# Kernel optimization log

Hardware: AMD Instinct MI355X
Metric: run time of the kernel (lower is better)

The kernel has to match this reference:

```python
import jax, jax.numpy as jnp
import numpy as np

H = 4      # SSM / attn heads (d_model/headdim = 256/64)
WIN = 4    # attention window over bands


def _ln(x, g, b):
    m = jnp.mean(x, -1, keepdims=True)
    v = jnp.mean((x - m) ** 2, -1, keepdims=True)
    return (x - m) * jax.lax.rsqrt(v + 1e-5) * g + b


def setup_inputs() -> dict:
    key = jax.random.key(0)
    ks = jax.random.split(key, 24)
    def rn(i, shape, s=0.05):
        return jax.random.normal(ks[i], shape, jnp.float32) * s
    B, T, K, D = 2, 256, 8, 256
    return {
        "z": rn(0, (B, T, K, D), 1.0),
        "ln1_g": jnp.ones((D,), jnp.float32), "ln1_b": jnp.zeros((D,), jnp.float32),
        "Wx": rn(1, (D, D)), "conv_w": rn(2, (D, 4), 0.3), "Wz": rn(3, (D, D)),
        "Wb": rn(4, (D, H * 128)), "Wc": rn(5, (D, H * 128)), "Wdt": rn(6, (D, H)),
        "dt_bias": rn(7, (H,), 0.5), "A_log": rn(8, (H,), 0.5), "theta": rn(9, (H,), 1.0),
        "D_skip": rn(10, (H,), 1.0), "mimo_U": rn(11, (H, H), 0.5), "mimo_V": rn(12, (H, H), 0.5),
        "Wout": rn(13, (D, D)),
        "ln2_g": jnp.ones((D,), jnp.float32), "ln2_b": jnp.zeros((D,), jnp.float32),
        "attn_in_w": rn(14, (3 * D, D)), "attn_in_b": rn(15, (3 * D,), 0.02),
        "attn_out_w": rn(16, (D, D)), "attn_out_b": jnp.zeros((D,), jnp.float32),
        "ln3_g": jnp.ones((D,), jnp.float32), "ln3_b": jnp.zeros((D,), jnp.float32),
        "Wg": rn(17, (D, 4 * D)), "Wu": rn(18, (D, 4 * D)), "Wd": rn(19, (4 * D, D)),
    }


def _forward(z, ln1_g, ln1_b, Wx, conv_w, Wz, Wb, Wc, Wdt, dt_bias, A_log, theta,
             D_skip, mimo_U, mimo_V, Wout, ln2_g, ln2_b, attn_in_w, attn_in_b,
             attn_out_w, attn_out_b, ln3_g, ln3_b, Wg, Wu, Wd):
    B, T, K, D = z.shape
    P = D // H
    N = Wb.shape[1] // H
    # ---------- (a) intra-band Mamba3 (complex MIMO selective scan) ----------
    u = _ln(z, ln1_g, ln1_b)
    u = jnp.transpose(u, (0, 2, 1, 3)).reshape(B * K, T, D)   # [BK,T,D]
    x = u @ Wx
    # causal depthwise conv1d, kernel 4
    xp = jnp.pad(x, ((0, 0), (3, 0), (0, 0)))
    x = sum(xp[:, k:k + T, :] * conv_w[:, k] for k in range(4))
    x = jax.nn.silu(x)
    xh = x.reshape(B * K, T, H, P)
    Bm = (u @ Wb).reshape(B * K, T, H, N)
    Cm = (u @ Wc).reshape(B * K, T, H, N)
    Mmix = mimo_U @ mimo_V.T                                  # rank-r cross-head coupling
    Bm = jnp.einsum('hg,btgn->bthn', Mmix, Bm)
    dt = jax.nn.softplus(u @ Wdt + dt_bias)                   # [BK,T,H]
    A = -jnp.exp(A_log)                                       # stable real decay
    mag = jnp.exp(dt * A)
    ph = dt * theta                                           # harmonic rotation
    ar, ai = mag * jnp.cos(ph), mag * jnp.sin(ph)
    xs = tuple(jnp.moveaxis(t, 1, 0) for t in (xh, Bm, Cm, dt, ar, ai))
    h0 = jnp.zeros((B * K, H, N, P), x.dtype)

    def step(carry, s):
        h_re, h_im = carry
        xt, bt, ct, dtt, art, ait = s
        dBx = (dtt[:, :, None, None] * bt[:, :, :, None]) * xt[:, :, None, :]
        nr = art[:, :, None, None] * h_re - ait[:, :, None, None] * h_im + dBx
        ni = art[:, :, None, None] * h_im + ait[:, :, None, None] * h_re
        return (nr, ni), jnp.einsum('bhn,bhnp->bhp', ct, nr)   # Re(C . h)

    _, ys = jax.lax.scan(step, (h0, h0), xs)                  # ys: [T,BK,H,P]
    y = jnp.moveaxis(ys, 0, 1) + D_skip[None, None, :, None] * xh
    y = y.reshape(B * K, T, D) * jax.nn.silu(u @ Wz)
    y = y @ Wout
    z = z + jnp.transpose(y.reshape(B, K, T, D), (0, 2, 1, 3))
    # ---------- (b) inter-band windowed attention ----------
    zn = _ln(z, ln2_g, ln2_b).reshape(B * T, K, D)
    qkv = zn @ attn_in_w.T + attn_in_b
    q, k_, v = jnp.split(qkv, 3, axis=-1)
    hd = D // H
    def hs(t):
        return t.reshape(B * T, K // WIN, WIN, H, hd).transpose(0, 1, 3, 2, 4)
    q, k_, v = hs(q), hs(k_), hs(v)
    s = jnp.einsum('mwhqd,mwhkd->mwhqk', q, k_) * jnp.float32(1.0 / np.sqrt(hd))
    a = jax.nn.softmax(s, axis=-1)
    o = jnp.einsum('mwhqk,mwhkd->mwhqd', a, v).transpose(0, 1, 3, 2, 4).reshape(B * T, K, D)
    z = z + (o @ attn_out_w.T + attn_out_b).reshape(B, T, K, D)
    # ---------- (c) SwiGLU FFN ----------
    zf = _ln(z, ln3_g, ln3_b)
    z = z + (jax.nn.silu(zf @ Wg) * (zf @ Wu)) @ Wd
    return z


def reference(z, ln1_g, ln1_b, Wx, conv_w, Wz, Wb, Wc, Wdt, dt_bias, A_log, theta,
              D_skip, mimo_U, mimo_V, Wout, ln2_g, ln2_b, attn_in_w, attn_in_b,
              attn_out_w, attn_out_b, ln3_g, ln3_b, Wg, Wu, Wd):
    return _forward(z, ln1_g, ln1_b, Wx, conv_w, Wz, Wb, Wc, Wdt, dt_bias, A_log,
                    theta, D_skip, mimo_U, mimo_V, Wout, ln2_g, ln2_b, attn_in_w,
                    attn_in_b, attn_out_w, attn_out_b, ln3_g, ln3_b, Wg, Wu, Wd)
```

## Files before the change

### kernel.cpp

```cpp
#include <hip/hip_runtime.h>
#include <hip/hip_bf16.h>
#include <math.h>

typedef __hip_bfloat16 bf16;
typedef __attribute__((ext_vector_type(8))) short s16x8;
typedef __attribute__((ext_vector_type(4))) float f32x4;

__device__ __forceinline__ float siluf(float x) { return x / (1.f + __expf(-x)); }
__device__ __forceinline__ float bits2f(unsigned short u) {
    union { float f; unsigned i; } v; v.i = ((unsigned)u) << 16; return v.f;
}
__device__ __forceinline__ unsigned short f2bits(float f) {
    return (unsigned short)__bfloat16_as_ushort(__float2bfloat16(f));
}

#define KFL 1024
#define OFF_UB   (768*KFL)
#define OFF_DTV  (1280*KFL)
#define OFF_BMB  (1344*KFL)
#define OFF_CMB  (2368*KFL)
#define OFF_ZGB  (3392*KFL)
#define OFF_XB   (3904*KFL)
#define OFF_X2T  (4928*KFL)
#define OFF_P    (5440*KFL)
#define OFF_YGB  (7488*KFL)
#define OFF_Z1   (8000*KFL)
#define OFF_ZNB  OFF_UB
#define OFF_QKV  OFF_BMB
#define OFF_OB   (2880*KFL)
#define OFF_Z2   OFF_P
#define OFF_ZFB  (6464*KFL)
#define OFF_GG   OFF_BMB

#define W_BCZX 0
#define W_OUT  393216
#define W_QKV  458752
#define W_AO   655360
#define W_GU   720896
#define W_D    1245184

__global__ __launch_bounds__(256) void prep_ln1_kernel(
    const float* __restrict__ Wx, const float* __restrict__ Wb,
    const float* __restrict__ Wc, const float* __restrict__ Wz,
    const float* __restrict__ Wo, const float* __restrict__ Wqkv,
    const float* __restrict__ Wao, const float* __restrict__ Wg,
    const float* __restrict__ Wu, const float* __restrict__ Wd,
    const float* __restrict__ U, const float* __restrict__ V,
    unsigned short* __restrict__ wout,
    const float* __restrict__ z, const float* __restrict__ g1,
    const float* __restrict__ b1, const float* __restrict__ Wdt,
    const float* __restrict__ dt_bias,
    unsigned short* __restrict__ u, float4* __restrict__ dtv4)
{
    __shared__ __align__(16) float smem[64 * 65];
    int blk = blockIdx.x;
    int tid = threadIdx.x;
    if (blk < 368) {
        if (blk >= 304) {
            int off = blk - 304;
            const float* src; int dst, base;
            if (off < 48) { src = Wqkv; dst = W_QKV; base = off * 4096; }
            else          { src = Wao;  dst = W_AO;  base = (off - 48) * 4096; }
            #pragma unroll
            for (int i = 0; i < 16; i++) {
                int idx = base + tid + i * 256;
                wout[dst + idx] = f2bits(src[idx]);
            }
            return;
        }
        float* lds = smem;
        const float* src; int srcN, n0, sc0, k0, dstoff, dstK, mix = 0, t;
        if (blk < 32)       { t = blk;       src = Wb; srcN = 512;  dstoff = W_BCZX; dstK = 256;
                              n0 = (t >> 2) * 64;        sc0 = 0; k0 = (t & 3) * 64; mix = 1; }
        else if (blk < 64)  { t = blk - 32;  src = Wc; srcN = 512;  dstoff = W_BCZX; dstK = 256;
                              n0 = 512 + (t >> 2) * 64;  sc0 = (t >> 2) * 64; k0 = (t & 3) * 64; }
        else if (blk < 80)  { t = blk - 64;  src = Wz; srcN = 256;  dstoff = W_BCZX; dstK = 256;
                              n0 = 1024 + (t >> 2) * 64; sc0 = (t >> 2) * 64; k0 = (t & 3) * 64; }
        else if (blk < 96)  { t = blk - 80;  src = Wx; srcN = 256;  dstoff = W_BCZX; dstK = 256;
                              n0 = 1280 + (t >> 2) * 64; sc0 = (t >> 2) * 64; k0 = (t & 3) * 64; }
        else if (blk < 112) { t = blk - 96;  src = Wo; srcN = 256;  dstoff = W_OUT;  dstK = 256;
                              n0 = (t >> 2) * 64;        sc0 = n0; k0 = (t & 3) * 64; }
        else if (blk < 176) { t = blk - 112; src = Wg; srcN = 1024; dstoff = W_GU;   dstK = 256;
                              n0 = (t >> 2) * 64;        sc0 = n0; k0 = (t & 3) * 64; }
        else if (blk < 240) { t = blk - 176; src = Wu; srcN = 1024; dstoff = W_GU;   dstK = 256;
                              n0 = 1024 + (t >> 2) * 64; sc0 = (t >> 2) * 64; k0 = (t & 3) * 64; }
        else                { t = blk - 240; src = Wd; srcN = 256;  dstoff = W_D;    dstK = 1024;
                              n0 = (t >> 4) * 64;        sc0 = n0; k0 = (t & 15) * 64; }
        if (mix) {
            int h = n0 >> 7, scol = n0 & 127;
            float mm[4];
            #pragma unroll
            for (int g = 0; g < 4; g++) {
                float s = 0.f;
                #pragma unroll
                for (int j = 0; j < 4; j++) s += U[h * 4 + j] * V[g * 4 + j];
                mm[g] = s;
            }
            #pragma unroll
            for (int i = 0; i < 16; i++) {
                int idx = tid + i * 256;
                int kk = idx >> 6, nn = idx & 63;
                const float* row = src + (size_t)(k0 + kk) * 512 + scol + nn;
                lds[kk * 65 + nn] = mm[0] * row[0] + mm[1] * row[128]
                                  + mm[2] * row[256] + mm[3] * row[384];
            }
        } else {
            #pragma unroll
            for (int i = 0; i < 16; i++) {
                int idx = tid + i * 256;
                int kk = idx >> 6, nn = idx & 63;
                lds[kk * 65 + nn] = src[(size_t)(k0 + kk) * srcN + sc0 + nn];
            }
        }
        __syncthreads();
// ... 268 lines not shown
            int s = bx * 128 + nwave + nf * 16 + lq;
            float ms = mAs[s];
            float ps = phs[s];
            float ds = dss[s];
            #pragma unroll
            for (int r = 0; r < 4; r++) {
                float wgt = (s <= tg[r])
                    ? __expf(tmv[r] - ms) * __cosf(tpv[r] - ps) * ds : 0.f;
                Pout[tg[r] * 256 + s] = f2bits(acc[mf][nf][r] * wgt);
            }
        }
    }
}

__global__ __launch_bounds__(256) void gemm_y(
    const unsigned short* __restrict__ P, const unsigned short* __restrict__ x2t,
    const unsigned short* __restrict__ zgb, const float* __restrict__ Dsk,
    unsigned short* __restrict__ ygb)
{
    int by = blockIdx.x, bh = blockIdx.y;
    int bk = bh >> 2, h = bh & 3;
    int tid = threadIdx.x;
    int w = tid >> 6, l = tid & 63;
    int mw = (w >> 1) * 32, nw = (w & 1) * 32;
    int lq = l & 15, lh = l >> 4;
    __shared__ __align__(16) unsigned short As[64 * 72];
    __shared__ __align__(16) unsigned short Bs[64 * 72];
    f32x4 acc[2][2] = {};
    int srow = tid >> 3, sc = (tid & 7) * 8;
    const unsigned short* Ap = P + (size_t)bh * 65536 + (size_t)(by * 64 + srow) * 256 + sc;
    const unsigned short* Bp = x2t + (size_t)bh * 16384 + (size_t)srow * 256 + sc;
    int kmax = (by + 1) * 64; if (kmax > 256) kmax = 256;
    uint4 a0 = *(const uint4*)(Ap);
    uint4 a1 = *(const uint4*)(Ap + (size_t)32 * 256);
    uint4 b0 = *(const uint4*)(Bp);
    uint4 b1 = *(const uint4*)(Bp + (size_t)32 * 256);
    for (int k0 = 0; k0 < kmax; k0 += 64) {
        if (k0) __syncthreads();
        *(uint4*)&As[srow * 72 + sc] = a0;
        *(uint4*)&As[(srow + 32) * 72 + sc] = a1;
        *(uint4*)&Bs[srow * 72 + sc] = b0;
        *(uint4*)&Bs[(srow + 32) * 72 + sc] = b1;
        __syncthreads();
        if (k0 + 64 < kmax) {
            a0 = *(const uint4*)(Ap + k0 + 64);
            a1 = *(const uint4*)(Ap + (size_t)32 * 256 + k0 + 64);
            b0 = *(const uint4*)(Bp + k0 + 64);
            b1 = *(const uint4*)(Bp + (size_t)32 * 256 + k0 + 64);
        }
        #pragma unroll
        for (int kk = 0; kk < 2; kk++) {
            int kof = kk * 32 + lh * 8;
            s16x8 bfr[2];
            #pragma unroll
            for (int nf = 0; nf < 2; nf++)
                bfr[nf] = *(const s16x8*)&Bs[(nw + nf * 16 + lq) * 72 + kof];
            #pragma unroll
            for (int mf = 0; mf < 2; mf++) {
                s16x8 af = *(const s16x8*)&As[(mw + mf * 16 + lq) * 72 + kof];
                #pragma unroll
                for (int nf = 0; nf < 2; nf++)
                    acc[mf][nf] = __builtin_amdgcn_mfma_f32_16x16x32_bf16(af, bfr[nf], acc[mf][nf], 0, 0, 0);
            }
        }
    }
    float dsk = Dsk[h];
    #pragma unroll
    for (int mf = 0; mf < 2; mf++) {
        #pragma unroll
        for (int nf = 0; nf < 2; nf++) {
            int p = nw + nf * 16 + lq;
            #pragma unroll
            for (int r = 0; r < 4; r++) {
                int t = by * 64 + mw + mf * 16 + lh * 4 + r;
                float xv = bits2f(x2t[(size_t)bh * 16384 + p * 256 + t]);
                float zg = bits2f(zgb[(size_t)(bk * 256 + t) * 256 + h * 64 + p]);
                ygb[(size_t)(bk * 256 + t) * 256 + h * 64 + p] =
                    f2bits((acc[mf][nf][r] + dsk * xv) * zg);
            }
        }
    }
}

__global__ __launch_bounds__(256) void gemm_ln(
    const unsigned short* __restrict__ A, const unsigned short* __restrict__ Bt,
    const float* __restrict__ bias, const float* __restrict__ resid,
    const float* __restrict__ g, const float* __restrict__ b,
    float* __restrict__ zfull, unsigned short* __restrict__ znorm, int rowmap)
{
    const int K = 256;
    __shared__ __align__(16) unsigned short As[16 * 72];
    __shared__ __align__(16) unsigned short Bs[256 * 72];
    __shared__ float partS[16][4], partQ[16][4];
    int tid = threadIdx.x;
    int m0 = blockIdx.x * 16;
    int w = tid >> 6, l = tid & 63;
    int nw = w * 64;
    int lq = l & 15, lh = l >> 4;
    f32x4 acc[4] = {};
    int srow = tid >> 3, sc = (tid & 7) * 8;
    const unsigned short* Ap = A + (size_t)(m0 + (srow & 15)) * K + sc;
    const unsigned short* Bp = Bt + (size_t)srow * K + sc;
    uint4 a0 = *(const uint4*)(Ap);
    uint4 b0 = *(const uint4*)(Bp);
    uint4 b1 = *(const uint4*)(Bp + (size_t)32 * K);
    uint4 b2 = *(const uint4*)(Bp + (size_t)64 * K);
    uint4 b3 = *(const uint4*)(Bp + (size_t)96 * K);
    uint4 b4 = *(const uint4*)(Bp + (size_t)128 * K);
    uint4 b5 = *(const uint4*)(Bp + (size_t)160 * K);
    uint4 b6 = *(const uint4*)(Bp + (size_t)192 * K);
    uint4 b7 = *(const uint4*)(Bp + (size_t)224 * K);
    for (int k0 = 0; k0 < K; k0 += 64) {
        if (k0) __syncthreads();
        if (tid < 128) *(uint4*)&As[srow * 72 + sc] = a0;
        *(uint4*)&Bs[srow * 72 + sc] = b0;
        *(uint4*)&Bs[(srow + 32) * 72 + sc] = b1;
        *(uint4*)&Bs[(srow + 64) * 72 + sc] = b2;
        *(uint4*)&Bs[(srow + 96) * 72 + sc] = b3;
        *(uint4*)&Bs[(srow + 128) * 72 + sc] = b4;
        *(uint4*)&Bs[(srow + 160) * 72 + sc] = b5;
        *(uint4*)&Bs[(srow + 192) * 72 + sc] = b6;
        *(uint4*)&Bs[(srow + 224) * 72 + sc] = b7;
        __syncthreads();
        if (k0 + 64 < K) {
            a0 = *(const uint4*)(Ap + k0 + 64);
            b0 = *(const uint4*)(Bp + k0 + 64);
            b1 = *(const uint4*)(Bp + (size_t)32 * K + k0 + 64);
            b2 = *(const uint4*)(Bp + (size_t)64 * K + k0 + 64);
            b3 = *(const uint4*)(Bp + (size_t)96 * K + k0 + 64);
            b4 = *(const uint4*)(Bp + (size_t)128 * K + k0 + 64);
            b5 = *(const uint4*)(Bp + (size_t)160 * K + k0 + 64);
            b6 = *(const uint4*)(Bp + (size_t)192 * K + k0 + 64);
            b7 = *(const uint4*)(Bp + (size_t)224 * K + k0 + 64);
        }
        #pragma unroll
        for (int kk = 0; kk < 2; kk++) {
            int kof = kk * 32 + lh * 8;
            s16x8 af = *(const s16x8*)&As[lq * 72 + kof];
            #pragma unroll
            for (int nf = 0; nf < 4; nf++) {
                s16x8 bf = *(const s16x8*)&Bs[(nw + nf * 16 + lq) * 72 + kof];
                acc[nf] = __builtin_amdgcn_mfma_f32_16x16x32_bf16(af, bf, acc[nf], 0, 0, 0);
            }
        }
    }
    float bv[4];
    #pragma unroll
    for (int nf = 0; nf < 4; nf++) bv[nf] = bias ? bias[nw + nf * 16 + lq] : 0.f;
    int orow[4];
    #pragma unroll
    for (int r = 0; r < 4; r++) {
        int rb = m0 + lh * 4 + r;
        if (rowmap) {
            int bk = rb >> 8, t = rb & 255;
            orow[r] = ((bk >> 3) * 256 + t) * 8 + (bk & 7);
        } else orow[r] = rb;
    }
    #pragma unroll
    for (int r = 0; r < 4; r++) {
        float s = 0.f, q = 0.f;
        #pragma unroll
        for (int nf = 0; nf < 4; nf++) {
            float v = acc[nf][r] + bv[nf]
                    + resid[(size_t)orow[r] * 256 + nw + nf * 16 + lq];
            acc[nf][r] = v;
            s += v; q += v * v;
        }
        #pragma unroll
        for (int off = 1; off < 16; off <<= 1) {
            s += __shfl_xor(s, off, 64);
            q += __shfl_xor(q, off, 64);
        }
        if (lq == 0) {
            int row = lh * 4 + r;
            partS[row][w] = s; partQ[row][w] = q;
        }
    }
    __syncthreads();
    float gv[4], bbv[4];
    #pragma unroll
    for (int nf = 0; nf < 4; nf++) {
        gv[nf] = g[nw + nf * 16 + lq];
        bbv[nf] = b[nw + nf * 16 + lq];
    }
    #pragma unroll
    for (int r = 0; r < 4; r++) {
        int row = lh * 4 + r;
        float sum = partS[row][0] + partS[row][1] + partS[row][2] + partS[row][3];
        float sq  = partQ[row][0] + partQ[row][1] + partQ[row][2] + partQ[row][3];
        float mean = sum * (1.f / 256.f);
        float var = sq * (1.f / 256.f) - mean * mean;
        float rstd = rsqrtf(var + 1e-5f);
        size_t ro = (size_t)orow[r] * 256;
        #pragma unroll
        for (int nf = 0; nf < 4; nf++) {
            int n = nw + nf * 16 + lq;
            float v = acc[nf][r];
            zfull[ro + n] = v;
            znorm[ro + n] = f2bits((v - mean) * rstd * gv[nf] + bbv[nf]);
        }
    }
}

__global__ __launch_bounds__(256) void mfma_gemm(
    const unsigned short* __restrict__ A, const unsigned short* __restrict__ Bt,
    const float* __restrict__ bias, void* __restrict__ C,
    int N, int K, int out_bf16)
{
    __shared__ __align__(16) unsigned short As[128 * 72];
    __shared__ __align__(16) unsigned short Bs[128 * 72];
    int tid = threadIdx.x;
    int n0 = blockIdx.x * 128, m0 = blockIdx.y * 128;
    int w = tid >> 6, l = tid & 63;
    int mwave = (w >> 1) * 64, nwave = (w & 1) * 64;
    f32x4 acc[4][4] = {};
    int srow = tid >> 3, sc = (tid & 7) * 8;
    const unsigned short* Ap = A + (size_t)(m0 + srow) * K + sc;
    const unsigned short* Bp = Bt + (size_t)(n0 + srow) * K + sc;
    int lq = l & 15, lh = l >> 4;
    uint4 a0 = *(const uint4*)(Ap);
    uint4 a1 = *(const uint4*)(Ap + (size_t)32 * K);
    uint4 a2 = *(const uint4*)(Ap + (size_t)64 * K);
    uint4 a3 = *(const uint4*)(Ap + (size_t)96 * K);
    uint4 b0 = *(const uint4*)(Bp);
    uint4 b1 = *(const uint4*)(Bp + (size_t)32 * K);
    uint4 b2 = *(const uint4*)(Bp + (size_t)64 * K);
    uint4 b3 = *(const uint4*)(Bp + (size_t)96 * K);
    for (int k0 = 0; k0 < K; k0 += 64) {
        if (k0) __syncthreads();
        *(uint4*)&As[srow * 72 + sc] = a0;
        *(uint4*)&As[(srow + 32) * 72 + sc] = a1;
        *(uint4*)&As[(srow + 64) * 72 + sc] = a2;
        *(uint4*)&As[(srow + 96) * 72 + sc] = a3;
        *(uint4*)&Bs[srow * 72 + sc] = b0;
        *(uint4*)&Bs[(srow + 32) * 72 + sc] = b1;
        *(uint4*)&Bs[(srow + 64) * 72 + sc] = b2;
        *(uint4*)&Bs[(srow + 96) * 72 + sc] = b3;
        __syncthreads();
        if (k0 + 64 < K) {
            a0 = *(const uint4*)(Ap + k0 + 64);
            a1 = *(const uint4*)(Ap + (size_t)32 * K + k0 + 64);
            a2 = *(const uint4*)(Ap + (size_t)64 * K + k0 + 64);
            a3 = *(const uint4*)(Ap + (size_t)96 * K + k0 + 64);
            b0 = *(const uint4*)(Bp + k0 + 64);
            b1 = *(const uint4*)(Bp + (size_t)32 * K + k0 + 64);
            b2 = *(const uint4*)(Bp + (size_t)64 * K + k0 + 64);
            b3 = *(const uint4*)(Bp + (size_t)96 * K + k0 + 64);
        }
        #pragma unroll
        for (int kk = 0; kk < 2; kk++) {
            int kof = kk * 32 + lh * 8;
            s16x8 bfr[4];
            #pragma unroll
            for (int nf = 0; nf < 4; nf++)
                bfr[nf] = *(const s16x8*)&Bs[(nwave + nf * 16 + lq) * 72 + kof];
            #pragma unroll
            for (int mf = 0; mf < 4; mf++) {
                s16x8 af = *(const s16x8*)&As[(mwave + mf * 16 + lq) * 72 + kof];
                #pragma unroll
                for (int nf = 0; nf < 4; nf++)
                    acc[mf][nf] = __builtin_amdgcn_mfma_f32_16x16x32_bf16(af, bfr[nf], acc[mf][nf], 0, 0, 0);
            }
        }
    }
    #pragma unroll
    for (int mf = 0; mf < 4; mf++) {
        #pragma unroll
        for (int nf = 0; nf < 4; nf++) {
            int n = n0 + nwave + nf * 16 + lq;
            float bs_ = bias ? bias[n] : 0.f;
            #pragma unroll
            for (int r = 0; r < 4; r++) {
                int m = m0 + mwave + mf * 16 + lh * 4 + r;
                float v = acc[mf][nf][r] + bs_;
                if (out_bf16) ((unsigned short*)C)[(size_t)m * N + n] = f2bits(v);
                else          ((float*)C)[(size_t)m * N + n] = v;
            }
        }
    }
}

__global__ __launch_bounds__(256) void gemm_gu2(
    const unsigned short* __restrict__ A, const unsigned short* __restrict__ Wgu,
    unsigned short* __restrict__ gg)
{
    const int K = 256;
    __shared__ __align__(16) unsigned short As[128 * 72];
    __shared__ __align__(16) unsigned short Bgs[64 * 72];
    __shared__ __align__(16) unsigned short Bus[64 * 72];
    int tid = threadIdx.x;
    int n0 = blockIdx.x * 64, m0 = blockIdx.y * 128;
    int w = tid >> 6, l = tid & 63;
    int mwave = (w >> 1) * 64, nwave = (w & 1) * 32;
    int lq = l & 15, lh = l >> 4;
    f32x4 ag[4][2] = {}, au[4][2] = {};
    int srow = tid >> 3, sc = (tid & 7) * 8;
    const unsigned short* Ap = A + (size_t)(m0 + srow) * K + sc;
    const unsigned short* Bgp = Wgu + (size_t)(n0 + srow) * K + sc;
    const unsigned short* Bup = Wgu + (size_t)(1024 + n0 + srow) * K + sc;
    uint4 a0 = *(const uint4*)(Ap);
    uint4 a1 = *(const uint4*)(Ap + (size_t)32 * K);
    uint4 a2 = *(const uint4*)(Ap + (size_t)64 * K);
    uint4 a3 = *(const uint4*)(Ap + (size_t)96 * K);
    uint4 bg0 = *(const uint4*)(Bgp);
    uint4 bg1 = *(const uint4*)(Bgp + (size_t)32 * K);
    uint4 bu0 = *(const uint4*)(Bup);
    uint4 bu1 = *(const uint4*)(Bup + (size_t)32 * K);
    for (int k0 = 0; k0 < K; k0 += 64) {
        if (k0) __syncthreads();
        *(uint4*)&As[srow * 72 + sc] = a0;
        *(uint4*)&As[(srow + 32) * 72 + sc] = a1;
        *(uint4*)&As[(srow + 64) * 72 + sc] = a2;
        *(uint4*)&As[(srow + 96) * 72 + sc] = a3;
        *(uint4*)&Bgs[srow * 72 + sc] = bg0;
        *(uint4*)&Bgs[(srow + 32) * 72 + sc] = bg1;
        *(uint4*)&Bus[srow * 72 + sc] = bu0;
        *(uint4*)&Bus[(srow + 32) * 72 + sc] = bu1;
        __syncthreads();
        if (k0 + 64 < K) {
            a0 = *(const uint4*)(Ap + k0 + 64);
            a1 = *(const uint4*)(Ap + (size_t)32 * K + k0 + 64);
            a2 = *(const uint4*)(Ap + (size_t)64 * K + k0 + 64);
            a3 = *(const uint4*)(Ap + (size_t)96 * K + k0 + 64);
            bg0 = *(const uint4*)(Bgp + k0 + 64);
            bg1 = *(const uint4*)(Bgp + (size_t)32 * K + k0 + 64);
            bu0 = *(const uint4*)(Bup + k0 + 64);
            bu1 = *(const uint4*)(Bup + (size_t)32 * K + k0 + 64);
        }
        #pragma unroll
        for (int kk = 0; kk < 2; kk++) {
            int kof = kk * 32 + lh * 8;
            s16x8 bgr[2], bur[2];
            #pragma unroll
            for (int nf = 0; nf < 2; nf++) {
                bgr[nf] = *(const s16x8*)&Bgs[(nwave + nf * 16 + lq) * 72 + kof];
                bur[nf] = *(const s16x8*)&Bus[(nwave + nf * 16 + lq) * 72 + kof];
            }
            #pragma unroll
            for (int mf = 0; mf < 4; mf++) {
                s16x8 af = *(const s16x8*)&As[(mwave + mf * 16 + lq) * 72 + kof];
                #pragma unroll
                for (int nf = 0; nf < 2; nf++) {
                    ag[mf][nf] = __builtin_amdgcn_mfma_f32_16x16x32_bf16(af, bgr[nf], ag[mf][nf], 0, 0, 0);
                    au[mf][nf] = __builtin_amdgcn_mfma_f32_16x16x32_bf16(af, bur[nf], au[mf][nf], 0, 0, 0);
                }
            }
        }
    }
    #pragma unroll
    for (int mf = 0; mf < 4; mf++) {
        #pragma unroll
        for (int nf = 0; nf < 2; nf++) {
            int n = n0 + nwave + nf * 16 + lq;
            #pragma unroll
            for (int r = 0; r < 4; r++) {
                int m = m0 + mwave + mf * 16 + lh * 4 + r;
                gg[(size_t)m * 1024 + n] = f2bits(siluf(ag[mf][nf][r]) * au[mf][nf][r]);
            }
        }
    }
}

__global__ __launch_bounds__(256) void gemm_d2(
    const unsigned short* __restrict__ gg, const unsigned short* __restrict__ Bt,
    const float* __restrict__ resid, float* __restrict__ out)
{
    __shared__ __align__(16) unsigned short As[64 * 72];
    __shared__ __align__(16) unsigned short Bs[64 * 72];
    const int K = 1024, N = 256;
    int tid = threadIdx.x;
    int n0 = blockIdx.x * 64, m0 = blockIdx.y * 64;
    int w = tid >> 6, l = tid & 63;
    int mw = (w >> 1) * 32, nw = (w & 1) * 32;
    f32x4 acc[2][2] = {};
    int srow = tid >> 3, sc = (tid & 7) * 8;
    const unsigned short* Ap = gg + (size_t)(m0 + srow) * K + sc;
    const unsigned short* Bp = Bt + (size_t)(n0 + srow) * K + sc;
    int lq = l & 15, lh = l >> 4;
    uint4 a0 = *(const uint4*)(Ap);
    uint4 a1 = *(const uint4*)(Ap + (size_t)32 * K);
    uint4 b0 = *(const uint4*)(Bp);
    uint4 b1 = *(const uint4*)(Bp + (size_t)32 * K);
    for (int k0 = 0; k0 < K; k0 += 64) {
        if (k0) __syncthreads();
        *(uint4*)&As[srow * 72 + sc] = a0;
        *(uint4*)&As[(srow + 32) * 72 + sc] = a1;
        *(uint4*)&Bs[srow * 72 + sc] = b0;
        *(uint4*)&Bs[(srow + 32) * 72 + sc] = b1;
        __syncthreads();
        if (k0 + 64 < K) {
            a0 = *(const uint4*)(Ap + k0 + 64);
            a1 = *(const uint4*)(Ap + (size_t)32 * K + k0 + 64);
            b0 = *(const uint4*)(Bp + k0 + 64);
            b1 = *(const uint4*)(Bp + (size_t)32 * K + k0 + 64);
        }
        #pragma unroll
        for (int kk = 0; kk < 2; kk++) {
            int kof = kk * 32 + lh * 8;
            s16x8 bfr[2];
            #pragma unroll
            for (int nf = 0; nf < 2; nf++)
                bfr[nf] = *(const s16x8*)&Bs[(nw + nf * 16 + lq) * 72 + kof];
            #pragma unroll
            for (int mf = 0; mf < 2; mf++) {
                s16x8 af = *(const s16x8*)&As[(mw + mf * 16 + lq) * 72 + kof];
                #pragma unroll
                for (int nf = 0; nf < 2; nf++)
                    acc[mf][nf] = __builtin_amdgcn_mfma_f32_16x16x32_bf16(af, bfr[nf], acc[mf][nf], 0, 0, 0);
            }
        }
    }
    #pragma unroll
    for (int mf = 0; mf < 2; mf++) {
        #pragma unroll
        for (int nf = 0; nf < 2; nf++) {
            int n = n0 + nw + nf * 16 + lq;
            #pragma unroll
            for (int r = 0; r < 4; r++) {
                int m = m0 + mw + mf * 16 + lh * 4 + r;
                out[(size_t)m * N + n] = acc[mf][nf][r] + resid[(size_t)m * N + n];
            }
        }
    }
}

__global__ __launch_bounds__(256) void attn_kernel(const unsigned short* __restrict__ qkv,
    unsigned short* __restrict__ o)
{
    int m = blockIdx.x >> 1, w = blockIdx.x & 1;
    int tid = threadIdx.x;
    int h = tid >> 6, d = tid & 63;
    __shared__ float qs[4][256], ks[4][256], vs[4][256];
    #pragma unroll
    for (int j = 0; j < 4; j++) {
        int row = m * 8 + w * 4 + j;
        int base = row * 768;
        qs[j][tid] = bits2f(qkv[base + tid]);
        ks[j][tid] = bits2f(qkv[base + 256 + tid]);
        vs[j][tid] = bits2f(qkv[base + 512 + tid]);
    }
    __syncthreads();
    float sc[4][4];
    #pragma unroll
    for (int qi = 0; qi < 4; qi++)
        #pragma unroll
        for (int ki = 0; ki < 4; ki++) {
            float v = qs[qi][h * 64 + d] * ks[ki][h * 64 + d];
            #pragma unroll
            for (int off = 32; off; off >>= 1) v += __shfl_xor(v, off, 64);
            sc[qi][ki] = v * 0.125f;
        }
    #pragma unroll
    for (int qi = 0; qi < 4; qi++) {
        float mx = fmaxf(fmaxf(sc[qi][0], sc[qi][1]), fmaxf(sc[qi][2], sc[qi][3]));
        float e0 = __expf(sc[qi][0] - mx), e1 = __expf(sc[qi][1] - mx);
        float e2 = __expf(sc[qi][2] - mx), e3 = __expf(sc[qi][3] - mx);
        float inv = 1.f / (e0 + e1 + e2 + e3);
        float ov = (e0 * vs[0][h * 64 + d] + e1 * vs[1][h * 64 + d] +
                    e2 * vs[2][h * 64 + d] + e3 * vs[3][h * 64 + d]) * inv;
        o[(m * 8 + w * 4 + qi) * 256 + h * 64 + d] = f2bits(ov);
    }
}

extern "C" void kernel_launch(void* const* d_in, const int* in_sizes, int n_in,
                              void* d_out, int out_size, void* d_ws, size_t ws_size,
                              hipStream_t stream)
{
    const float* z         = (const float*)d_in[0];
    const float* ln1_g     = (const float*)d_in[1];
    const float* ln1_b     = (const float*)d_in[2];
    const float* Wx        = (const float*)d_in[3];
    const float* conv_w    = (const float*)d_in[4];
    const float* Wz        = (const float*)d_in[5];
    const float* Wb        = (const float*)d_in[6];
    const float* Wc        = (const float*)d_in[7];
    const float* Wdt       = (const float*)d_in[8];
    const float* dt_bias   = (const float*)d_in[9];
    const float* A_log     = (const float*)d_in[10];
    const float* theta     = (const float*)d_in[11];
    const float* D_skip    = (const float*)d_in[12];
    const float* mimo_U    = (const float*)d_in[13];
    const float* mimo_V    = (const float*)d_in[14];
    const float* Wout      = (const float*)d_in[15];
    const float* ln2_g     = (const float*)d_in[16];
    const float* ln2_b     = (const float*)d_in[17];
    const float* attn_in_w = (const float*)d_in[18];
    const float* attn_in_b = (const float*)d_in[19];
    const float* attn_out_w= (const float*)d_in[20];
    const float* attn_out_b= (const float*)d_in[21];
    const float* ln3_g     = (const float*)d_in[22];
    const float* ln3_b     = (const float*)d_in[23];
    const float* Wg        = (const float*)d_in[24];
    const float* Wu        = (const float*)d_in[25];
    const float* Wd        = (const float*)d_in[26];

    float* W = (float*)d_ws;
    unsigned short* wts = (unsigned short*)W;
    unsigned short* ub  = (unsigned short*)(W + OFF_UB);
    float4* dtv4        = (float4*)(W + OFF_DTV);
    unsigned short* bmb = (unsigned short*)(W + OFF_BMB);
    unsigned short* cmb = (unsigned short*)(W + OFF_CMB);
    unsigned short* zgb = (unsigned short*)(W + OFF_ZGB);
    unsigned short* xb  = (unsigned short*)(W + OFF_XB);
    unsigned short* x2t = (unsigned short*)(W + OFF_X2T);
    unsigned short* pbuf= (unsigned short*)(W + OFF_P);
    unsigned short* ygb = (unsigned short*)(W + OFF_YGB);
    float* z1           = W + OFF_Z1;
    unsigned short* znb = (unsigned short*)(W + OFF_ZNB);
    unsigned short* qkvb= (unsigned short*)(W + OFF_QKV);
    unsigned short* ob  = (unsigned short*)(W + OFF_OB);
    float* z2           = W + OFF_Z2;
    unsigned short* zfb = (unsigned short*)(W + OFF_ZFB);
    unsigned short* gg  = (unsigned short*)(W + OFF_GG);

    prep_ln1_kernel<<<4464, 256, 0, stream>>>(
        Wx, Wb, Wc, Wz, Wout, attn_in_w, attn_out_w, Wg, Wu, Wd, mimo_U, mimo_V,
        wts, z, ln1_g, ln1_b, Wdt, dt_bias, ub, dtv4);
    gemm_bczx<<<dim3(12, 32), 256, 0, stream>>>(ub, wts + W_BCZX, bmb, cmb, zgb, xb);
    s_conv_kernel<<<448, 256, 0, stream>>>(cmb, bmb, dtv4, A_log, theta, pbuf,
                                           xb, conv_w, x2t);
    gemm_y<<<dim3(4, 64), 256, 0, stream>>>(pbuf, x2t, zgb, D_skip, ygb);
    gemm_ln<<<256, 256, 0, stream>>>(ygb, wts + W_OUT, nullptr, z, ln2_g, ln2_b,
                                     z1, znb, 1);
    mfma_gemm<<<dim3(6, 32), 256, 0, stream>>>(znb, wts + W_QKV, attn_in_b, qkvb, 768, 256, 1);
    attn_kernel<<<1024, 256, 0, stream>>>(qkvb, ob);
    gemm_ln<<<256, 256, 0, stream>>>(ob, wts + W_AO, attn_out_b, z1, ln3_g, ln3_b,
                                     z2, zfb, 0);
    gemm_gu2<<<dim3(16, 32), 256, 0, stream>>>(zfb, wts + W_GU, gg);
    gemm_d2<<<dim3(4, 64), 256, 0, stream>>>(gg, wts + W_D, z2, (float*)d_out);
}
```

Measured before the change: 209.9 us.

## Fuse out-proj, LN2, QKV GEMM, band attention, attn-out and LN3 into one kernel

Replaces four launches (gemm_ln, mfma_gemm, attn_kernel, gemm_ln) with one mid_kernel. Each block owns 16 rows, which are two full 8-band tokens, so the windowed attention can run entirely in shared memory. The row permutation moves from the output side to the input gather. This removes the global round trips for z1, the normalized activations, qkv and the attention output, plus three launch gaps. In exchange it uses about 63KB of shared memory per block and runs only 256 blocks, each doing five serialized weight-streaming GEMM passes with many barriers, so occupancy and parallelism drop.

```diff
diff --git a/kernel.cpp b/kernel.cpp
--- a/kernel.cpp
+++ b/kernel.cpp
@@ -24,12 +24,8 @@
 #define OFF_X2T  (4928*KFL)
 #define OFF_P    (5440*KFL)
 #define OFF_YGB  (7488*KFL)
-#define OFF_Z1   (8000*KFL)
-#define OFF_ZNB  OFF_UB
-#define OFF_QKV  OFF_BMB
-#define OFF_OB   (2880*KFL)
-#define OFF_Z2   OFF_P
-#define OFF_ZFB  (6464*KFL)
+#define OFF_Z2   (8000*KFL)
+#define OFF_ZFB  (9024*KFL)
 #define OFF_GG   OFF_BMB
 
 #define W_BCZX 0
@@ -464,199 +460,306 @@
     }
 }
 
-__global__ __launch_bounds__(256) void gemm_ln(
-    const unsigned short* __restrict__ A, const unsigned short* __restrict__ Bt,
-    const float* __restrict__ bias, const float* __restrict__ resid,
-    const float* __restrict__ g, const float* __restrict__ b,
-    float* __restrict__ zfull, unsigned short* __restrict__ znorm, int rowmap)
+__global__ __launch_bounds__(256) void mid_kernel(
+    const unsigned short* __restrict__ ygb, const unsigned short* __restrict__ wts,
+    const float* __restrict__ zin,
+    const float* __restrict__ g2, const float* __restrict__ b2,
+    const float* __restrict__ qbias, const float* __restrict__ obias,
+    const float* __restrict__ g3, const float* __restrict__ b3,
+    float* __restrict__ z2, unsigned short* __restrict__ zfb)
 {
+    __shared__ __align__(16) char smem[64512];
+    unsigned short* Bs = (unsigned short*)smem;
+    unsigned short* As = (unsigned short*)(smem + 36864);
+    unsigned short* zn = (unsigned short*)(smem + 39168);
+    float* z1s = (float*)(smem + 47616);
+    float (*partS)[4] = (float(*)[4])(smem + 64000);
+    float (*partQ)[4] = (float(*)[4])(smem + 64256);
+    unsigned short* qk = (unsigned short*)smem;
+
     const int K = 256;
-    __shared__ __align__(16) unsigned short As[16 * 72];
-    __shared__ __align__(16) unsigned short Bs[256 * 72];
-    __shared__ float partS[16][4], partQ[16][4];
     int tid = threadIdx.x;
     int m0 = blockIdx.x * 16;
     int w = tid >> 6, l = tid & 63;
     int nw = w * 64;
     int lq = l & 15, lh = l >> 4;
-    f32x4 acc[4] = {};
     int srow = tid >> 3, sc = (tid & 7) * 8;
-    const unsigned short* Ap = A + (size_t)(m0 + (srow & 15)) * K + sc;
-    const unsigned short* Bp = Bt + (size_t)srow * K + sc;
-    uint4 a0 = *(const uint4*)(Ap);
-    uint4 b0 = *(const uint4*)(Bp);
-    uint4 b1 = *(const uint4*)(Bp + (size_t)32 * K);
-    uint4 b2 = *(const uint4*)(Bp + (size_t)64 * K);
-    uint4 b3 = *(const uint4*)(Bp + (size_t)96 * K);
-    uint4 b4 = *(const uint4*)(Bp + (size_t)128 * K);
-    uint4 b5 = *(const uint4*)(Bp + (size_t)160 * K);
-    uint4 b6 = *(const uint4*)(Bp + (size_t)192 * K);
-    uint4 b7 = *(const uint4*)(Bp + (size_t)224 * K);
-    for (int k0 = 0; k0 < K; k0 += 64) {
-        if (k0) __syncthreads();
-        if (tid < 128) *(uint4*)&As[srow * 72 + sc] = a0;
-        *(uint4*)&Bs[srow * 72 + sc] = b0;
-        *(uint4*)&Bs[(srow + 32) * 72 + sc] = b1;
-        *(uint4*)&Bs[(srow + 64) * 72 + sc] = b2;
-        *(uint4*)&Bs[(srow + 96) * 72 + sc] = b3;
-        *(uint4*)&Bs[(srow + 128) * 72 + sc] = b4;
-        *(uint4*)&Bs[(srow + 160) * 72 + sc] = b5;
-        *(uint4*)&Bs[(srow + 192) * 72 + sc] = b6;
-        *(uint4*)&Bs[(srow + 224) * 72 + sc] = b7;
-        __syncthreads();
-        if (k0 + 64 < K) {
-            a0 = *(const uint4*)(Ap + k0 + 64);
-            b0 = *(const uint4*)(Bp + k0 + 64);
-            b1 = *(const uint4*)(Bp + (size_t)32 * K + k0 + 64);
-            b2 = *(const uint4*)(Bp + (size_t)64 * K + k0 + 64);
-            b3 = *(const uint4*)(Bp + (size_t)96 * K + k0 + 64);
-            b4 = *(const uint4*)(Bp + (size_t)128 * K + k0 + 64);
-            b5 = *(const uint4*)(Bp + (size_t)160 * K + k0 + 64);
-            b6 = *(const uint4*)(Bp + (size_t)192 * K + k0 + 64);
-            b7 = *(const uint4*)(Bp + (size_t)224 * K + k0 + 64);
-        }
-        #pragma unroll
-        for (int kk = 0; kk < 2; kk++) {
-            int kof = kk * 32 + lh * 8;
-            s16x8 af = *(const s16x8*)&As[lq * 72 + kof];
+
+    {
+        int rb = m0 + (srow & 15);
+        int irow = ((rb >> 11) * 8 + (rb & 7)) * 256 + ((rb >> 3) & 255);
+        const unsigned short* Ap = ygb + (size_t)irow * K + sc;
+        const unsigned short* Bp = wts + W_OUT + (size_t)srow * K + sc;
+        f32x4 acc[4] = {};
+        uint4 a0 = *(const uint4*)(Ap);
+        uint4 c0 = *(const uint4*)(Bp);
+        uint4 c1 = *(const uint4*)(Bp + (size_t)32 * K);
+        uint4 c2 = *(const uint4*)(Bp + (size_t)64 * K);
+        uint4 c3 = *(const uint4*)(Bp + (size_t)96 * K);
+        uint4 c4 = *(const uint4*)(Bp + (size_t)128 * K);
+        uint4 c5 = *(const uint4*)(Bp + (size_t)160 * K);
+        uint4 c6 = *(const uint4*)(Bp + (size_t)192 * K);
+        uint4 c7 = *(const uint4*)(Bp + (size_t)224 * K);
+        for (int k0 = 0; k0 < K; k0 += 64) {
+            if (k0) __syncthreads();
+            if (tid < 128) *(uint4*)&As[srow * 72 + sc] = a0;
+            *(uint4*)&Bs[srow * 72 + sc] = c0;
+            *(uint4*)&Bs[(srow + 32) * 72 + sc] = c1;
+            *(uint4*)&Bs[(srow + 64) * 72 + sc] = c2;
+            *(uint4*)&Bs[(srow + 96) * 72 + sc] = c3;
+            *(uint4*)&Bs[(srow + 128) * 72 + sc] = c4;
+            *(uint4*)&Bs[(srow + 160) * 72 + sc] = c5;
+            *(uint4*)&Bs[(srow + 192) * 72 + sc] = c6;
+            *(uint4*)&Bs[(srow + 224) * 72 + sc] = c7;
+            __syncthreads();
+            if (k0 + 64 < K) {
+                a0 = *(const uint4*)(Ap + k0 + 64);
+                c0 = *(const uint4*)(Bp + k0 + 64);
+                c1 = *(const uint4*)(Bp + (size_t)32 * K + k0 + 64);
+                c2 = *(const uint4*)(Bp + (size_t)64 * K + k0 + 64);
+                c3 = *(const uint4*)(Bp + (size_t)96 * K + k0 + 64);
+                c4 = *(const uint4*)(Bp + (size_t)128 * K + k0 + 64);
+                c5 = *(const uint4*)(Bp + (size_t)160 * K + k0 + 64);
+                c6 = *(const uint4*)(Bp + (size_t)192 * K + k0 + 64);
+                c7 = *(const uint4*)(Bp + (size_t)224 * K + k0 + 64);
+            }
+            #pragma unroll
+            for (int kk = 0; kk < 2; kk++) {
+                int kof = kk * 32 + lh * 8;
+                s16x8 af = *(const s16x8*)&As[lq * 72 + kof];
+                #pragma unroll
+                for (int nf = 0; nf < 4; nf++) {
+                    s16x8 bf = *(const s16x8*)&Bs[(nw + nf * 16 + lq) * 72 + kof];
+                    acc[nf] = __builtin_amdgcn_mfma_f32_16x16x32_bf16(af, bf, acc[nf], 0, 0, 0);
+                }
+            }
+        }
+        #pragma unroll
+        for (int r = 0; r < 4; r++) {
+            int row = lh * 4 + r;
+            float s = 0.f, q = 0.f;
             #pragma unroll
             for (int nf = 0; nf < 4; nf++) {
-                s16x8 bf = *(const s16x8*)&Bs[(nw + nf * 16 + lq) * 72 + kof];
-                acc[nf] = __builtin_amdgcn_mfma_f32_16x16x32_bf16(af, bf, acc[nf], 0, 0, 0);
-            }
-        }
-    }
-    float bv[4];
-    #pragma unroll
-    for (int nf = 0; nf < 4; nf++) bv[nf] = bias ? bias[nw + nf * 16 + lq] : 0.f;
-    int orow[4];
-    #pragma unroll
-    for (int r = 0; r < 4; r++) {
-        int rb = m0 + lh * 4 + r;
-        if (rowmap) {
-            int bk = rb >> 8, t = rb & 255;
-            orow[r] = ((bk >> 3) * 256 + t) * 8 + (bk & 7);
-        } else orow[r] = rb;
-    }
-    #pragma unroll
-    for (int r = 0; r < 4; r++) {
-        float s = 0.f, q = 0.f;
+                float v = acc[nf][r] + zin[(size_t)(m0 + row) * 256 + nw + nf * 16 + lq];
+                acc[nf][r] = v;
+                s += v; q += v * v;
+            }
+            #pragma unroll
+            for (int off = 1; off < 16; off <<= 1) {
+                s += __shfl_xor(s, off, 64);
+                q += __shfl_xor(q, off, 64);
+            }
+            if (lq == 0) { partS[row][w] = s; partQ[row][w] = q; }
+        }
+        __syncthreads();
+        float gv[4], bbv[4];
         #pragma unroll
         for (int nf = 0; nf < 4; nf++) {
-            float v = acc[nf][r] + bv[nf]
-                    + resid[(size_t)orow[r] * 256 + nw + nf * 16 + lq];
-            acc[nf][r] = v;
-            s += v; q += v * v;
-        }
-        #pragma unroll
-        for (int off = 1; off < 16; off <<= 1) {
-            s += __shfl_xor(s, off, 64);
-            q += __shfl_xor(q, off, 64);
-        }
-        if (lq == 0) {
+            gv[nf] = g2[nw + nf * 16 + lq];
+            bbv[nf] = b2[nw + nf * 16 + lq];
+        }
+        #pragma unroll
+        for (int r = 0; r < 4; r++) {
             int row = lh * 4 + r;
-            partS[row][w] = s; partQ[row][w] = q;
-        }
-    }
+            float sum = partS[row][0] + partS[row][1] + partS[row][2] + partS[row][3];
+            float sq  = partQ[row][0] + partQ[row][1] + partQ[row][2] + partQ[row][3];
+            float mean = sum * (1.f / 256.f);
+            float var = sq * (1.f / 256.f) - mean * mean;
+            float rstd = rsqrtf(var + 1e-5f);
+            #pragma unroll
+            for (int nf = 0; nf < 4; nf++) {
+                int n = nw + nf * 16 + lq;
+                float v = acc[nf][r];
+                z1s[row * 256 + n] = v;
+                zn[row * 264 + n] = f2bits((v - mean) * rstd * gv[nf] + bbv[nf]);
+            }
+        }
+    }
+
+    f32x4 aq0[4] = {}, aq1[4] = {}, aq2[4] = {};
+#define QKV_PASS(PIDX, AQ) do { \
+    const unsigned short* Bp2 = wts + W_QKV + (size_t)((PIDX) * 256 + srow) * 256 + sc; \
+    uint4 d0 = *(const uint4*)(Bp2); \
+    uint4 d1 = *(const uint4*)(Bp2 + (size_t)32 * 256); \
+    uint4 d2 = *(const uint4*)(Bp2 + (size_t)64 * 256); \
+    uint4 d3 = *(const uint4*)(Bp2 + (size_t)96 * 256); \
+    uint4 d4 = *(const uint4*)(Bp2 + (size_t)128 * 256); \
+    uint4 d5 = *(const uint4*)(Bp2 + (size_t)160 * 256); \
+    uint4 d6 = *(const uint4*)(Bp2 + (size_t)192 * 256); \
+    uint4 d7 = *(const uint4*)(Bp2 + (size_t)224 * 256); \
+    for (int k0 = 0; k0 < 256; k0 += 64) { \
+        __syncthreads(); \
+        *(uint4*)&Bs[srow * 72 + sc] = d0; \
+        *(uint4*)&Bs[(srow + 32) * 72 + sc] = d1; \
+        *(uint4*)&Bs[(srow + 64) * 72 + sc] = d2; \
+        *(uint4*)&Bs[(srow + 96) * 72 + sc] = d3; \
+        *(uint4*)&Bs[(srow + 128) * 72 + sc] = d4; \
+        *(uint4*)&Bs[(srow + 160) * 72 + sc] = d5; \
+        *(uint4*)&Bs[(srow + 192) * 72 + sc] = d6; \
+        *(uint4*)&Bs[(srow + 224) * 72 + sc] = d7; \
+        __syncthreads(); \
+        if (k0 + 64 < 256) { \
+            d0 = *(const uint4*)(Bp2 + k0 + 64); \
+            d1 = *(const uint4*)(Bp2 + (size_t)32 * 256 + k0 + 64); \
+            d2 = *(const uint4*)(Bp2 + (size_t)64 * 256 + k0 + 64); \
+            d3 = *(const uint4*)(Bp2 + (size_t)96 * 256 + k0 + 64); \
+            d4 = *(const uint4*)(Bp2 + (size_t)128 * 256 + k0 + 64); \
+            d5 = *(const uint4*)(Bp2 + (size_t)160 * 256 + k0 + 64); \
+            d6 = *(const uint4*)(Bp2 + (size_t)192 * 256 + k0 + 64); \
+            d7 = *(const uint4*)(Bp2 + (size_t)224 * 256 + k0 + 64); \
+        } \
+        _Pragma("unroll") \
+        for (int kk = 0; kk < 2; kk++) { \
+            int kof = kk * 32 + lh * 8; \
+            s16x8 af = *(const s16x8*)&zn[lq * 264 + k0 + kof]; \
+            _Pragma("unroll") \
+            for (int nf = 0; nf < 4; nf++) { \
+                s16x8 bf = *(const s16x8*)&Bs[(nw + nf * 16 + lq) * 72 + kof]; \
+                AQ[nf] = __builtin_amdgcn_mfma_f32_16x16x32_bf16(af, bf, AQ[nf], 0, 0, 0); \
+            } \
+        } \
+    } \
+} while (0)
+    QKV_PASS(0, aq0);
+    QKV_PASS(1, aq1);
+    QKV_PASS(2, aq2);
+#undef QKV_PASS
+
     __syncthreads();
-    float gv[4], bbv[4];
-    #pragma unroll
-    for (int nf = 0; nf < 4; nf++) {
-        gv[nf] = g[nw + nf * 16 + lq];
-        bbv[nf] = b[nw + nf * 16 + lq];
-    }
-    #pragma unroll
-    for (int r = 0; r < 4; r++) {
-        int row = lh * 4 + r;
-        float sum = partS[row][0] + partS[row][1] + partS[row][2] + partS[row][3];
-        float sq  = partQ[row][0] + partQ[row][1] + partQ[row][2] + partQ[row][3];
-        float mean = sum * (1.f / 256.f);
-        float var = sq * (1.f / 256.f) - mean * mean;
-        float rstd = rsqrtf(var + 1e-5f);
-        size_t ro = (size_t)orow[r] * 256;
+#define QKV_STORE(PIDX, AQ) do { \
+    _Pragma("unroll") \
+    for (int nf = 0; nf < 4; nf++) { \
+        int n = (PIDX) * 256 + nw + nf * 16 + lq; \
+        float bb = qbias[n]; \
+        _Pragma("unroll") \
+        for (int r = 0; r < 4; r++) \
+            qk[(lh * 4 + r) * 776 + n] = f2bits(AQ[nf][r] + bb); \
+    } \
+} while (0)
+    QKV_STORE(0, aq0);
+    QKV_STORE(1, aq1);
+    QKV_STORE(2, aq2);
+#undef QKV_STORE
+    __syncthreads();
+    {
+        int hh = w;
+        int d = l;
+        #pragma unroll
+        for (int w4 = 0; w4 < 4; w4++) {
+            int r0 = w4 * 4;
+            float qv[4], kv[4], vv[4];
+            #pragma unroll
+            for (int j = 0; j < 4; j++) {
+                qv[j] = bits2f(qk[(r0 + j) * 776 + hh * 64 + d]);
+                kv[j] = bits2f(qk[(r0 + j) * 776 + 256 + hh * 64 + d]);
+                vv[j] = bits2f(qk[(r0 + j) * 776 + 512 + hh * 64 + d]);
+            }
+            float sc_[4][4];
+            #pragma unroll
+            for (int qi = 0; qi < 4; qi++)
+                #pragma unroll
+                for (int ki = 0; ki < 4; ki++) {
+                    float v = qv[qi] * kv[ki];
+                    #pragma unroll
+                    for (int off = 32; off; off >>= 1) v += __shfl_xor(v, off, 64);
+                    sc_[qi][ki] = v * 0.125f;
+                }
+            #pragma unroll
+            for (int qi = 0; qi < 4; qi++) {
+                float mx = fmaxf(fmaxf(sc_[qi][0], sc_[qi][1]), fmaxf(sc_[qi][2], sc_[qi][3]));
+                float e0 = __expf(sc_[qi][0] - mx), e1 = __expf(sc_[qi][1] - mx);
+                float e2 = __expf(sc_[qi][2] - mx), e3 = __expf(sc_[qi][3] - mx);
+                float inv = 1.f / (e0 + e1 + e2 + e3);
+                float ov = (e0 * vv[0] + e1 * vv[1] + e2 * vv[2] + e3 * vv[3]) * inv;
+                zn[(r0 + qi) * 264 + hh * 64 + d] = f2bits(ov);
+            }
+        }
+    }
+
+    {
+        f32x4 ac4[4] = {};
+        const unsigned short* Bp4 = wts + W_AO + (size_t)srow * K + sc;
+        uint4 c0 = *(const uint4*)(Bp4);
+        uint4 c1 = *(const uint4*)(Bp4 + (size_t)32 * K);
+        uint4 c2 = *(const uint4*)(Bp4 + (size_t)64 * K);
+        uint4 c3 = *(const uint4*)(Bp4 + (size_t)96 * K);
+        uint4 c4 = *(const uint4*)(Bp4 + (size_t)128 * K);
+        uint4 c5 = *(const uint4*)(Bp4 + (size_t)160 * K);
+        uint4 c6 = *(const uint4*)(Bp4 + (size_t)192 * K);
+        uint4 c7 = *(const uint4*)(Bp4 + (size_t)224 * K);
+        for (int k0 = 0; k0 < K; k0 += 64) {
+            __syncthreads();
+            *(uint4*)&Bs[srow * 72 + sc] = c0;
+            *(uint4*)&Bs[(srow + 32) * 72 + sc] = c1;
+            *(uint4*)&Bs[(srow + 64) * 72 + sc] = c2;
+            *(uint4*)&Bs[(srow + 96) * 72 + sc] = c3;
+            *(uint4*)&Bs[(srow + 128) * 72 + sc] = c4;
+            *(uint4*)&Bs[(srow + 160) * 72 + sc] = c5;
+            *(uint4*)&Bs[(srow + 192) * 72 + sc] = c6;
+            *(uint4*)&Bs[(srow + 224) * 72 + sc] = c7;
+            __syncthreads();
+            if (k0 + 64 < K) {
+                c0 = *(const uint4*)(Bp4 + k0 + 64);
+                c1 = *(const uint4*)(Bp4 + (size_t)32 * K + k0 + 64);
+                c2 = *(const uint4*)(Bp4 + (size_t)64 * K + k0 + 64);
+                c3 = *(const uint4*)(Bp4 + (size_t)96 * K + k0 + 64);
+                c4 = *(const uint4*)(Bp4 + (size_t)128 * K + k0 + 64);
+                c5 = *(const uint4*)(Bp4 + (size_t)160 * K + k0 + 64);
+                c6 = *(const uint4*)(Bp4 + (size_t)192 * K + k0 + 64);
+                c7 = *(const uint4*)(Bp4 + (size_t)224 * K + k0 + 64);
+            }
+            #pragma unroll
+            for (int kk = 0; kk < 2; kk++) {
+                int kof = kk * 32 + lh * 8;
+                s16x8 af = *(const s16x8*)&zn[lq * 264 + k0 + kof];
+                #pragma unroll
+                for (int nf = 0; nf < 4; nf++) {
+                    s16x8 bf = *(const s16x8*)&Bs[(nw + nf * 16 + lq) * 72 + kof];
+                    ac4[nf] = __builtin_amdgcn_mfma_f32_16x16x32_bf16(af, bf, ac4[nf], 0, 0, 0);
+                }
+            }
+        }
+        float bv[4], gv[4], bbv[4];
         #pragma unroll
         for (int nf = 0; nf < 4; nf++) {
             int n = nw + nf * 16 + lq;
-            float v = acc[nf][r];
-            zfull[ro + n] = v;
-            znorm[ro + n] = f2bits((v - mean) * rstd * gv[nf] + bbv[nf]);
-        }
-    }
-}
-
-__global__ __launch_bounds__(256) void mfma_gemm(
-    const unsigned short* __restrict__ A, const unsigned short* __restrict__ Bt,
-    const float* __restrict__ bias, void* __restrict__ C,
-    int N, int K, int out_bf16)
-{
-    __shared__ __align__(16) unsigned short As[128 * 72];
-    __shared__ __align__(16) unsigned short Bs[128 * 72];
-    int tid = threadIdx.x;
-    int n0 = blockIdx.x * 128, m0 = blockIdx.y * 128;
-    int w = tid >> 6, l = tid & 63;
-    int mwave = (w >> 1) * 64, nwave = (w & 1) * 64;
-    f32x4 acc[4][4] = {};
-    int srow = tid >> 3, sc = (tid & 7) * 8;
-    const unsigned short* Ap = A + (size_t)(m0 + srow) * K + sc;
-    const unsigned short* Bp = Bt + (size_t)(n0 + srow) * K + sc;
-    int lq = l & 15, lh = l >> 4;
-    uint4 a0 = *(const uint4*)(Ap);
-    uint4 a1 = *(const uint4*)(Ap + (size_t)32 * K);
-    uint4 a2 = *(const uint4*)(Ap + (size_t)64 * K);
-    uint4 a3 = *(const uint4*)(Ap + (size_t)96 * K);
-    uint4 b0 = *(const uint4*)(Bp);
-    uint4 b1 = *(const uint4*)(Bp + (size_t)32 * K);
-    uint4 b2 = *(const uint4*)(Bp + (size_t)64 * K);
-    uint4 b3 = *(const uint4*)(Bp + (size_t)96 * K);
-    for (int k0 = 0; k0 < K; k0 += 64) {
-        if (k0) __syncthreads();
-        *(uint4*)&As[srow * 72 + sc] = a0;
-        *(uint4*)&As[(srow + 32) * 72 + sc] = a1;
-        *(uint4*)&As[(srow + 64) * 72 + sc] = a2;
-        *(uint4*)&As[(srow + 96) * 72 + sc] = a3;
-        *(uint4*)&Bs[srow * 72 + sc] = b0;
-        *(uint4*)&Bs[(srow + 32) * 72 + sc] = b1;
-        *(uint4*)&Bs[(srow + 64) * 72 + sc] = b2;
-        *(uint4*)&Bs[(srow + 96) * 72 + sc] = b3;
-        __syncthreads();
-        if (k0 + 64 < K) {
-            a0 = *(const uint4*)(Ap + k0 + 64);
-            a1 = *(const uint4*)(Ap + (size_t)32 * K + k0 + 64);
-            a2 = *(const uint4*)(Ap + (size_t)64 * K + k0 + 64);
-            a3 = *(const uint4*)(Ap + (size_t)96 * K + k0 + 64);
-            b0 = *(const uint4*)(Bp + k0 + 64);
-            b1 = *(const uint4*)(Bp + (size_t)32 * K + k0 + 64);
-            b2 = *(const uint4*)(Bp + (size_t)64 * K + k0 + 64);
-            b3 = *(const uint4*)(Bp + (size_t)96 * K + k0 + 64);
-        }
-        #pragma unroll
-        for (int kk = 0; kk < 2; kk++) {
-            int kof = kk * 32 + lh * 8;
-            s16x8 bfr[4];
-            #pragma unroll
-            for (int nf = 0; nf < 4; nf++)
-                bfr[nf] = *(const s16x8*)&Bs[(nwave + nf * 16 + lq) * 72 + kof];
-            #pragma unroll
-            for (int mf = 0; mf < 4; mf++) {
-                s16x8 af = *(const s16x8*)&As[(mwave + mf * 16 + lq) * 72 + kof];
-                #pragma unroll
-                for (int nf = 0; nf < 4; nf++)
-                    acc[mf][nf] = __builtin_amdgcn_mfma_f32_16x16x32_bf16(af, bfr[nf], acc[mf][nf], 0, 0, 0);
-            }
-        }
-    }
-    #pragma unroll
-    for (int mf = 0; mf < 4; mf++) {
-        #pragma unroll
-        for (int nf = 0; nf < 4; nf++) {
-            int n = n0 + nwave + nf * 16 + lq;
-            float bs_ = bias ? bias[n] : 0.f;
-            #pragma unroll
-            for (int r = 0; r < 4; r++) {
-                int m = m0 + mwave + mf * 16 + lh * 4 + r;
-                float v = acc[mf][nf][r] + bs_;
-                if (out_bf16) ((unsigned short*)C)[(size_t)m * N + n] = f2bits(v);
-                else          ((float*)C)[(size_t)m * N + n] = v;
+            bv[nf] = obias[n];
+            gv[nf] = g3[n];
+            bbv[nf] = b3[n];
+        }
+        #pragma unroll
+        for (int r = 0; r < 4; r++) {
+            int row = lh * 4 + r;
+            float s = 0.f, q = 0.f;
+            #pragma unroll
+            for (int nf = 0; nf < 4; nf++) {
+                float v = ac4[nf][r] + bv[nf] + z1s[row * 256 + nw + nf * 16 + lq];
+                ac4[nf][r] = v;
+                s += v; q += v * v;
+            }
+            #pragma unroll
+            for (int off = 1; off < 16; off <<= 1) {
+                s += __shfl_xor(s, off, 64);
+                q += __shfl_xor(q, off, 64);
+            }
+            if (lq == 0) { partS[row][w] = s; partQ[row][w] = q; }
+        }
+        __syncthreads();
+        #pragma unroll
+        for (int r = 0; r < 4; r++) {
+            int row = lh * 4 + r;
+            float sum = partS[row][0] + partS[row][1] + partS[row][2] + partS[row][3];
+            float sq  = partQ[row][0] + partQ[row][1] + partQ[row][2] + partQ[row][3];
+            float mean = sum * (1.f / 256.f);
+            float var = sq * (1.f / 256.f) - mean * mean;
+            float rstd = rsqrtf(var + 1e-5f);
+            size_t ro = (size_t)(m0 + row) * 256;
+            #pragma unroll
+            for (int nf = 0; nf < 4; nf++) {
+                int n = nw + nf * 16 + lq;
+                float v = ac4[nf][r];
+                z2[ro + n] = v;
+                zfb[ro + n] = f2bits((v - mean) * rstd * gv[nf] + bbv[nf]);
             }
         }
     }
@@ -806,44 +909,6 @@
     }
 }
 
-__global__ __launch_bounds__(256) void attn_kernel(const unsigned short* __restrict__ qkv,
-    unsigned short* __restrict__ o)
-{
-    int m = blockIdx.x >> 1, w = blockIdx.x & 1;
-    int tid = threadIdx.x;
-    int h = tid >> 6, d = tid & 63;
-    __shared__ float qs[4][256], ks[4][256], vs[4][256];
-    #pragma unroll
-    for (int j = 0; j < 4; j++) {
-        int row = m * 8 + w * 4 + j;
-        int base = row * 768;
-        qs[j][tid] = bits2f(qkv[base + tid]);
-        ks[j][tid] = bits2f(qkv[base + 256 + tid]);
-        vs[j][tid] = bits2f(qkv[base + 512 + tid]);
-    }
-    __syncthreads();
-    float sc[4][4];
-    #pragma unroll
-    for (int qi = 0; qi < 4; qi++)
-        #pragma unroll
-        for (int ki = 0; ki < 4; ki++) {
-            float v = qs[qi][h * 64 + d] * ks[ki][h * 64 + d];
-            #pragma unroll
-            for (int off = 32; off; off >>= 1) v += __shfl_xor(v, off, 64);
-            sc[qi][ki] = v * 0.125f;
-        }
-    #pragma unroll
-    for (int qi = 0; qi < 4; qi++) {
-        float mx = fmaxf(fmaxf(sc[qi][0], sc[qi][1]), fmaxf(sc[qi][2], sc[qi][3]));
-        float e0 = __expf(sc[qi][0] - mx), e1 = __expf(sc[qi][1] - mx);
-        float e2 = __expf(sc[qi][2] - mx), e3 = __expf(sc[qi][3] - mx);
-        float inv = 1.f / (e0 + e1 + e2 + e3);
-        float ov = (e0 * vs[0][h * 64 + d] + e1 * vs[1][h * 64 + d] +
-                    e2 * vs[2][h * 64 + d] + e3 * vs[3][h * 64 + d]) * inv;
-        o[(m * 8 + w * 4 + qi) * 256 + h * 64 + d] = f2bits(ov);
-    }
-}
-
 extern "C" void kernel_launch(void* const* d_in, const int* in_sizes, int n_in,
                               void* d_out, int out_size, void* d_ws, size_t ws_size,
                               hipStream_t stream)
@@ -887,10 +952,6 @@
     unsigned short* x2t = (unsigned short*)(W + OFF_X2T);
     unsigned short* pbuf= (unsigned short*)(W + OFF_P);
     unsigned short* ygb = (unsigned short*)(W + OFF_YGB);
-    float* z1           = W + OFF_Z1;
-    unsigned short* znb = (unsigned short*)(W + OFF_ZNB);
-    unsigned short* qkvb= (unsigned short*)(W + OFF_QKV);
-    unsigned short* ob  = (unsigned short*)(W + OFF_OB);
     float* z2           = W + OFF_Z2;
     unsigned short* zfb = (unsigned short*)(W + OFF_ZFB);
     unsigned short* gg  = (unsigned short*)(W + OFF_GG);
@@ -902,12 +963,9 @@
     s_conv_kernel<<<448, 256, 0, stream>>>(cmb, bmb, dtv4, A_log, theta, pbuf,
                                            xb, conv_w, x2t);
     gemm_y<<<dim3(4, 64), 256, 0, stream>>>(pbuf, x2t, zgb, D_skip, ygb);
-    gemm_ln<<<256, 256, 0, stream>>>(ygb, wts + W_OUT, nullptr, z, ln2_g, ln2_b,
-                                     z1, znb, 1);
-    mfma_gemm<<<dim3(6, 32), 256, 0, stream>>>(znb, wts + W_QKV, attn_in_b, qkvb, 768, 256, 1);
-    attn_kernel<<<1024, 256, 0, stream>>>(qkvb, ob);
-    gemm_ln<<<256, 256, 0, stream>>>(ob, wts + W_AO, attn_out_b, z1, ln3_g, ln3_b,
-                                     z2, zfb, 0);
+    mid_kernel<<<256, 256, 0, stream>>>(ygb, wts, z, ln2_g, ln2_b,
+                                        attn_in_b, attn_out_b, ln3_g, ln3_b,
+                                        z2, zfb);
     gemm_gu2<<<dim3(16, 32), 256, 0, stream>>>(zfb, wts + W_GU, gg);
     gemm_d2<<<dim3(4, 64), 256, 0, stream>>>(gg, wts + W_D, z2, (float*)d_out);
 }
```

Result: faster. 198.6 us (-5.4%).
